# Optimization experiments

Measured on AMD Instinct MI355X. Metric: run time of the kernel, lower is better.

## Reference

```python
import jax, jax.numpy as jnp
import numpy as np


def setup_inputs() -> dict:
    key = jax.random.key(0)
    ks = jax.random.split(key, 7)
    B, C, H, W = 8, 256, 128, 128
    Cq = C // 8  # reduction_factor = 8
    x = jax.random.normal(ks[0], (B, C, H, W), jnp.float32)
    Wq = jax.random.normal(ks[1], (Cq, C), jnp.float32) * 0.05
    bq = jax.random.normal(ks[2], (Cq,), jnp.float32) * 0.01
    Wk = jax.random.normal(ks[3], (Cq, C), jnp.float32) * 0.05
    bk = jax.random.normal(ks[4], (Cq,), jnp.float32) * 0.01
    Wv = jax.random.normal(ks[5], (C, C), jnp.float32) * 0.05
    bv = jax.random.normal(ks[6], (C,), jnp.float32) * 0.01
    gamma = jnp.ones((1,), jnp.float32) * 0.5  # nonzero so attention path is active
    return {"x": x, "Wq": Wq, "bq": bq, "Wk": Wk, "bk": bk, "Wv": Wv, "bv": bv, "gamma": gamma}


def reference(x, Wq, bq, Wk, bk, Wv, bv, gamma):
    # 1x1 convs == per-pixel channel projections
    q = jnp.einsum('bchw,oc->bohw', x, Wq) + bq[None, :, None, None]  # [B,Cq,H,W]
    k = jnp.einsum('bchw,oc->bohw', x, Wk) + bk[None, :, None, None]
    v = jnp.einsum('bchw,oc->bohw', x, Wv) + bv[None, :, None, None]  # [B,C,H,W]

    H = x.shape[2]
    eye = jnp.eye(H, dtype=x.dtype)  # additive identity self-mask (note: +1, per source)

    # column (height) attention: for each (b, w), attend along h
    logit_h = jnp.einsum('bciw,bcjw->bwij', q, k) + eye  # [B,W,H,H]
    att_h = jax.nn.softmax(logit_h, axis=-1)
    out_h = jnp.einsum('bwij,bcjw->bciw', att_h, v)  # [B,C,H,W]

    # row (width) attention: for each (b, h), attend along w
    logit_w = jnp.einsum('bchi,bchj->bhij', q, k)  # [B,H,W,W]
    att_w = jax.nn.softmax(logit_w, axis=-1)
    out_w = jnp.einsum('bhij,bchj->bchi', att_w, v)  # [B,C,H,W]

    return gamma[0] * (out_h + out_w) + x
```

## Files before the change

kernel.cpp:

```cpp
#include <hip/hip_runtime.h>
#include <hip/hip_bf16.h>

#define BN 8
#define CN 256
#define CQn 32
#define HN 128
#define WN 128
#define LST 132

using bf16 = __hip_bfloat16;
typedef short short8 __attribute__((ext_vector_type(8)));
typedef float f32x4 __attribute__((ext_vector_type(4)));

__device__ __forceinline__ float ldf(const float* p) { return *p; }
__device__ __forceinline__ float ldf(const bf16* p) { return __bfloat162float(*p); }
__device__ __forceinline__ void stf(float* p, float v) { *p = v; }
__device__ __forceinline__ void stf(bf16* p, float v) { *p = __float2bfloat16(v); }
__device__ __forceinline__ unsigned short f2bu(float v) {
  bf16 h = __float2bfloat16(v);
  return *(unsigned short*)&h;
}
__device__ __forceinline__ float bu2f(unsigned short u) {
  return __bfloat162float(*(const bf16*)&u);
}
__device__ __forceinline__ unsigned pack2(float a, float b) {
  return (unsigned)f2bu(a) | ((unsigned)f2bu(b) << 16);
}
__device__ __forceinline__ uint4 add8bf16(uint4 a, uint4 b) {
  union { uint4 v; unsigned short u[8]; } A, B, C;
  A.v = a; B.v = b;
#pragma unroll
  for (int e = 0; e < 8; ++e) C.u[e] = f2bu(bu2f(A.u[e]) + bu2f(B.u[e]));
  return C.v;
}


__global__ __launch_bounds__(256) void proj_qk2(
    const float* __restrict__ x, const float* __restrict__ Wq, const float* __restrict__ bq,
    const float* __restrict__ Wk, const float* __restrict__ bk,
    bf16* __restrict__ qF, bf16* __restrict__ kF) {
  __shared__ float xs[64][128];
  __shared__ float wqs[CQn][64];
  __shared__ float wks[CQn][64];
  __shared__ float bqs[CQn], bks[CQn];
  const int tid = threadIdx.x;
  const int b = blockIdx.x >> 7, h = blockIdx.x & 127;
  if (tid < CQn) { bqs[tid] = bq[tid]; bks[tid] = bk[tid]; }
  const int w0 = (tid & 63) * 2;
  const int g = tid >> 6;
  float accq[8][2] = {};
  float acck[8][2] = {};
  for (int cc = 0; cc < CN; cc += 64) {
    __syncthreads();
    for (int idx = tid; idx < 64 * 128; idx += 256) {
      int c = idx >> 7, ww = idx & 127;
      xs[c][ww] = x[(((size_t)b * CN + cc + c) * HN + h) * WN + ww];
    }
    for (int idx = tid; idx < CQn * 64; idx += 256) {
      int oc = idx >> 6, c = idx & 63;
      wqs[oc][c] = Wq[oc * CN + cc + c];
      wks[oc][c] = Wk[oc * CN + cc + c];
    }
    __syncthreads();
    for (int c4 = 0; c4 < 64; c4 += 4) {
      float xa[4][2];
#pragma unroll
      for (int a = 0; a < 4; ++a) {
        float2 v = *(const float2*)&xs[c4 + a][w0];
        xa[a][0] = v.x; xa[a][1] = v.y;
      }
#pragma unroll
      for (int r = 0; r < 8; ++r) {
        float4 wq4 = *(const float4*)&wqs[g * 8 + r][c4];
        float4 wk4 = *(const float4*)&wks[g * 8 + r][c4];
        float wqa[4] = {wq4.x, wq4.y, wq4.z, wq4.w};
        float wka[4] = {wk4.x, wk4.y, wk4.z, wk4.w};
#pragma unroll
        for (int a = 0; a < 4; ++a) {
          accq[r][0] += wqa[a] * xa[a][0];
          accq[r][1] += wqa[a] * xa[a][1];
          acck[r][0] += wka[a] * xa[a][0];
          acck[r][1] += wka[a] * xa[a][1];
        }
      }
    }
  }
#pragma unroll
  for (int e = 0; e < 2; ++e) {
    union { unsigned short u[8]; uint4 v; } pq, pk;
#pragma unroll
    for (int rr = 0; rr < 8; ++rr) {
      int oc = g * 8 + rr;
      pq.u[rr] = f2bu(accq[rr][e] + bqs[oc]);
      pk.u[rr] = f2bu(acck[rr][e] + bks[oc]);
    }
    size_t base = (((size_t)b * 128 + h) * 128 + (w0 + e)) * 32 + g * 8;
    *(uint4*)&qF[base] = pq.v;
    *(uint4*)&kF[base] = pk.v;
  }
}

template <bool COL>
__global__ __launch_bounds__(256) void attn_mfma(
    const bf16* __restrict__ qF, const bf16* __restrict__ kF,
    const void* __restrict__ vsrc, bf16* __restrict__ outP) {
  __shared__ unsigned short psm[128 * 128];
  __shared__ float rsum[128];
  const int tid = threadIdx.x;
  const int wid = tid >> 6;
  const int lane = tid & 63;
  const int l15 = lane & 15, lg = lane >> 4;
  const int b = blockIdx.x >> 7, r = blockIdx.x & 127;

  short8 qf[2];
  const int ti0 = wid * 2;
#pragma unroll
  for (int t2 = 0; t2 < 2; ++t2) {
    int i = (ti0 + t2) * 16 + l15;
    size_t base = COL ? (((size_t)b * 128 + i) * 128 + r) * 32
                      : (((size_t)b * 128 + r) * 128 + i) * 32;
    qf[t2] = *(const short8*)&qF[base + lg * 8];
  }
  f32x4 lgt[2][8];
#pragma unroll
  for (int t2 = 0; t2 < 2; ++t2)
#pragma unroll
    for (int tj = 0; tj < 8; ++tj)
#pragma unroll
      for (int e = 0; e < 4; ++e) lgt[t2][tj][e] = 0.f;
#pragma unroll
  for (int tj = 0; tj < 8; ++tj) {
    int j = tj * 16 + l15;
    size_t base = COL ? (((size_t)b * 128 + j) * 128 + r) * 32
                      : (((size_t)b * 128 + r) * 128 + j) * 32;
    short8 kf = *(const short8*)&kF[base + lg * 8];
#pragma unroll
    for (int t2 = 0; t2 < 2; ++t2)
      lgt[t2][tj] = __builtin_amdgcn_mfma_f32_16x16x32_bf16(kf, qf[t2], lgt[t2][tj], 0, 0, 0);
  }

#pragma unroll
  for (int t2 = 0; t2 < 2; ++t2) {
    const int i = (ti0 + t2) * 16 + l15;
    if (COL) {
#pragma unroll
      for (int tj = 0; tj < 8; ++tj)
#pragma unroll
        for (int rr = 0; rr < 4; ++rr)
          if (tj * 16 + lg * 4 + rr == i) lgt[t2][tj][rr] += 1.0f;
    }
    float m = -1e30f;
#pragma unroll
    for (int tj = 0; tj < 8; ++tj)
#pragma unroll
      for (int rr = 0; rr < 4; ++rr) m = fmaxf(m, lgt[t2][tj][rr]);
    m = fmaxf(m, __shfl_xor(m, 16, 64));
    m = fmaxf(m, __shfl_xor(m, 32, 64));
    float s = 0.f;
#pragma unroll
    for (int tj = 0; tj < 8; ++tj)
#pragma unroll
      for (int rr = 0; rr < 4; ++rr) {
        float e = __expf(lgt[t2][tj][rr] - m);
        lgt[t2][tj][rr] = e;
        s += e;
      }
    s += __shfl_xor(s, 16, 64);
    s += __shfl_xor(s, 32, 64);
    if (lg == 0) rsum[i] = s;
#pragma unroll
    for (int tj = 0; tj < 8; ++tj) {
      int slot = ((tj * 2) + (lg >> 1)) ^ (i & 7);
      int elem = i * 128 + slot * 8 + (lg & 1) * 4;
      uint2 v;
      v.x = pack2(lgt[t2][tj][0], lgt[t2][tj][1]);
      v.y = pack2(lgt[t2][tj][2], lgt[t2][tj][3]);
      *(uint2*)&psm[elem] = v;
    }
  }
  __syncthreads();

  float rinv[8];
#pragma unroll
  for (int nt = 0; nt < 8; ++nt) rinv[nt] = 1.0f / rsum[nt * 16 + l15];

  const int cbase = wid * 64;
  const float* xf = (const float*)vsrc;
  const bf16* xb = (const bf16*)vsrc;
  unsigned short* ou = (unsigned short*)outP;
#pragma unroll
  for (int cp = 0; cp < 2; ++cp) {
    short8 vf[2][4];
#pragma unroll
    for (int u = 0; u < 2; ++u) {
      int c = cbase + (cp * 2 + u) * 16 + l15;
#pragma unroll
      for (int ks = 0; ks < 4; ++ks) {
        if (COL) {
          vf[u][ks] = *(const short8*)&xb[(((size_t)b * 256 + c) * 128 + r) * 128 + ks * 32 + lg * 8];
        } else {
          const float* xp = &xf[((size_t)b * 256 + c) * 16384 + r * 128 + ks * 32 + lg * 8];
          float4 f0 = *(const float4*)xp;
          float4 f1 = *(const float4*)(xp + 4);
          union { unsigned short u16[8]; short8 s8; } tmp;
          tmp.u16[0] = f2bu(f0.x); tmp.u16[1] = f2bu(f0.y);
          tmp.u16[2] = f2bu(f0.z); tmp.u16[3] = f2bu(f0.w);
          tmp.u16[4] = f2bu(f1.x); tmp.u16[5] = f2bu(f1.y);
          tmp.u16[6] = f2bu(f1.z); tmp.u16[7] = f2bu(f1.w);
          vf[u][ks] = tmp.s8;
        }
      }
    }
    f32x4 acc[2][8];
#pragma unroll
    for (int u = 0; u < 2; ++u)
#pragma unroll
      for (int nt = 0; nt < 8; ++nt)
#pragma unroll
        for (int e = 0; e < 4; ++e) acc[u][nt][e] = 0.f;
#pragma unroll
    for (int ks = 0; ks < 4; ++ks)
#pragma unroll
      for (int nt = 0; nt < 8; ++nt) {
        int i = nt * 16 + l15;
        short8 pf = *(const short8*)&psm[i * 128 + (((ks * 4) + lg) ^ (i & 7)) * 8];
#pragma unroll
        for (int u = 0; u < 2; ++u)
          acc[u][nt] = __builtin_amdgcn_mfma_f32_16x16x32_bf16(vf[u][ks], pf, acc[u][nt], 0, 0, 0);
      }
#pragma unroll
    for (int u = 0; u < 2; ++u) {
      int ct = cp * 2 + u;
      int cg = wid * 8 + ct * 2 + (lg >> 1);
#pragma unroll
      for (int nt = 0; nt < 8; ++nt) {
        int i = nt * 16 + l15;
        float sc = rinv[nt];
        uint2 v;
        v.x = pack2(acc[u][nt][0] * sc, acc[u][nt][1] * sc);
        v.y = pack2(acc[u][nt][2] * sc, acc[u][nt][3] * sc);
        size_t elem = ((((size_t)b * 32 + cg) * 128 + r) * 128 + i) * 8 + (lg & 1) * 4;
        *(uint2*)&ou[elem] = v;
      }
    }
  }
}

__global__ __launch_bounds__(256) void packed_merge2(const bf16* __restrict__ thP,
                                                     bf16* __restrict__ twP) {
  __shared__ uint4 ts[32][33];
  const int tid = threadIdx.x;
  const int blk = blockIdx.x;
  const int tI = blk & 15;
  const int cg = (blk >> 4) & 31;
  const int b = blk >> 9;
  const int h0 = (tI >> 2) * 32, w0 = (tI & 3) * 32;
  const uint4* tp = (const uint4*)thP;
  uint4* tw = (uint4*)twP;
#pragma unroll
  for (int rep = 0; rep < 4; ++rep) {
    int cell = rep * 256 + tid;
    int ww = cell >> 5, hh = cell & 31;
    ts[ww][hh] = tp[(((size_t)b * 32 + cg) * 128 + (w0 + ww)) * 128 + (h0 + hh)];
  }
  __syncthreads();
#pragma unroll
  for (int rep = 0; rep < 4; ++rep) {
    int cell = rep * 256 + tid;
    int hh = cell >> 5, ww = cell & 31;
    size_t o = (((size_t)b * 32 + cg) * 128 + (h0 + hh)) * 128 + (w0 + ww);
    tw[o] = add8bf16(tw[o], ts[ww][hh]);
  }
}


template <typename TIn>
__global__ __launch_bounds__(256) void transpose_bf16(const TIn* __restrict__ in,
                                                      bf16* __restrict__ out) {
  __shared__ float tile[32][33];
  const int blk = blockIdx.x;
  const int p = blk >> 4, t = blk & 15;
  const int r0 = (t >> 2) * 32, c0 = (t & 3) * 32;
  const int tx = threadIdx.x & 31, ty = threadIdx.x >> 5;
  const TIn* ip = in + (size_t)p * 128 * 128;
#pragma unroll
  for (int rr = 0; rr < 4; ++rr)
    tile[ty + 8 * rr][tx] = ldf(&ip[(r0 + ty + 8 * rr) * 128 + c0 + tx]);
  __syncthreads();
  bf16* op = out + (size_t)p * 128 * 128;
#pragma unroll
  for (int rr = 0; rr < 4; ++rr)
    op[(c0 + ty + 8 * rr) * 128 + r0 + tx] = __float2bfloat16(tile[tx][ty + 8 * rr]);
}

__global__ __launch_bounds__(256) void wv_to_bf16(const float* __restrict__ Wv,
                                                  bf16* __restrict__ Wvb) {
  int i = blockIdx.x * 256 + threadIdx.x;
  Wvb[i] = __float2bfloat16(Wv[i]);
}

__global__ __launch_bounds__(256) void proj_qk(
    const float* __restrict__ x, const float* __restrict__ Wq, const float* __restrict__ bq,
    const float* __restrict__ Wk, const float* __restrict__ bk,
    bf16* __restrict__ q, bf16* __restrict__ k) {
  __shared__ float xs[64][128];
  __shared__ float wqs[CQn][64];
  __shared__ float wks[CQn][64];
  __shared__ float bqs[CQn], bks[CQn];
  const int tid = threadIdx.x;
  const int b = blockIdx.x >> 7, h = blockIdx.x & 127;
  if (tid < CQn) { bqs[tid] = bq[tid]; bks[tid] = bk[tid]; }
  const int w0 = (tid & 63) * 2;
  const int g = tid >> 6;
  float accq[8][2] = {};
  float acck[8][2] = {};
  for (int cc = 0; cc < CN; cc += 64) {
    __syncthreads();
    for (int idx = tid; idx < 64 * 128; idx += 256) {
      int c = idx >> 7, ww = idx & 127;
      xs[c][ww] = x[(((size_t)b * CN + cc + c) * HN + h) * WN + ww];
    }
    for (int idx = tid; idx < CQn * 64; idx += 256) {
      int oc = idx >> 6, c = idx & 63;
      wqs[oc][c] = Wq[oc * CN + cc + c];
      wks[oc][c] = Wk[oc * CN + cc + c];
    }
    __syncthreads();
    for (int c4 = 0; c4 < 64; c4 += 4) {
      float xa[4][2];
#pragma unroll
      for (int a = 0; a < 4; ++a) {
        float2 v = *(const float2*)&xs[c4 + a][w0];
        xa[a][0] = v.x; xa[a][1] = v.y;
      }
#pragma unroll
      for (int r = 0; r < 8; ++r) {
        float4 wq4 = *(const float4*)&wqs[g * 8 + r][c4];
        float4 wk4 = *(const float4*)&wks[g * 8 + r][c4];
        float wqa[4] = {wq4.x, wq4.y, wq4.z, wq4.w};
        float wka[4] = {wk4.x, wk4.y, wk4.z, wk4.w};
#pragma unroll
        for (int a = 0; a < 4; ++a) {
          accq[r][0] += wqa[a] * xa[a][0];
          accq[r][1] += wqa[a] * xa[a][1];
          acck[r][0] += wka[a] * xa[a][0];
          acck[r][1] += wka[a] * xa[a][1];
        }
      }
    }
  }
#pragma unroll
  for (int r = 0; r < 8; ++r) {
    int oc = g * 8 + r;
    size_t off = (((size_t)b * CQn + oc) * HN + h) * WN + w0;
    q[off]     = __float2bfloat16(accq[r][0] + bqs[oc]);
    q[off + 1] = __float2bfloat16(accq[r][1] + bqs[oc]);
    k[off]     = __float2bfloat16(acck[r][0] + bks[oc]);
    k[off + 1] = __float2bfloat16(acck[r][1] + bks[oc]);
  }
}

template <typename XT, typename OT, bool ADD_EYE, bool PACKED>
__global__ __launch_bounds__(256) void attn_1d(
    const bf16* __restrict__ qsrc, const bf16* __restrict__ ksrc,
    const XT* __restrict__ xsrc, OT* __restrict__ outp) {
  extern __shared__ float sm[];
  float* qs  = sm;
  float* ks  = sm + 4096;
  float* Ls  = sm + 8192;
  float* xsv = sm + 8192 + 128 * LST;
  float* red = sm + 8192 + 160 * LST;
  float* rsum = sm + 8192 + 160 * LST + 256;
  const int tid = threadIdx.x;
  const int b = blockIdx.x >> 7, r = blockIdx.x & 127;

  for (int idx = tid; idx < CQn * 128; idx += 256) {
    int c = idx >> 7, j = idx & 127;
    size_t off = (((size_t)b * CQn + c) * 128 + r) * 128 + j;
    qs[idx] = __bfloat162float(qsrc[off]);
    ks[idx] = __bfloat162float(ksrc[off]);
  }
  __syncthreads();
#pragma unroll
  for (int g = 0; g < 4; ++g) {
    int t = tid + g * 256;
    int i0 = (t >> 5) * 4, j0 = (t & 31) * 4;
    float acc[4][4] = {};
    for (int c = 0; c < CQn; ++c) {
      float4 qv = *(const float4*)&qs[c * 128 + i0];
      float4 kv = *(const float4*)&ks[c * 128 + j0];
      float qa[4] = {qv.x, qv.y, qv.z, qv.w};
      float ka[4] = {kv.x, kv.y, kv.z, kv.w};
#pragma unroll
      for (int ii = 0; ii < 4; ++ii)
#pragma unroll
        for (int jj = 0; jj < 4; ++jj) acc[ii][jj] += qa[ii] * ka[jj];
    }
#pragma unroll
    for (int ii = 0; ii < 4; ++ii) {
      if (ADD_EYE) {
        int i = i0 + ii;
        if (i >= j0 && i < j0 + 4) acc[ii][i - j0] += 1.0f;
      }
      float4 o = make_float4(acc[ii][0], acc[ii][1], acc[ii][2], acc[ii][3]);
      *(float4*)&Ls[(i0 + ii) * LST + j0] = o;
    }
  }
  __syncthreads();
  {
    const int row = tid & 127, jb = (tid >> 7) * 64;
    float m = -1e30f;
    for (int j = 0; j < 64; ++j) m = fmaxf(m, Ls[row * LST + jb + j]);
    red[tid] = m;
    __syncthreads();
    m = fmaxf(red[row], red[row + 128]);
    float s = 0.f;
    for (int j = 0; j < 64; ++j) {
      float e = __expf(Ls[row * LST + jb + j] - m);
      Ls[row * LST + jb + j] = e;
      s += e;
    }
    __syncthreads();
    red[tid] = s;
    __syncthreads();
    if (tid < 128) rsum[tid] = red[tid] + red[tid + 128];
  }
  const int ci0 = (tid >> 5) * 4;
  const int il = tid & 31;
  float rinv[4];
  __syncthreads();
#pragma unroll
  for (int a = 0; a < 4; ++a) rinv[a] = 1.0f / rsum[il + 32 * a];

  for (int cc0 = 0; cc0 < CN; cc0 += 32) {
    __syncthreads();
    for (int idx = tid; idx < 32 * 128; idx += 256) {
      int c = idx >> 7, j = idx & 127;
      xsv[c * LST + j] = ldf(&xsrc[(((size_t)b * CN + cc0 + c) * 128 + r) * 128 + j]);
    }
    __syncthreads();
    float acc[4][4] = {};
    for (int j0 = 0; j0 < 128; j0 += 4) {
      float xa[4][4], pa[4][4];
#pragma unroll
      for (int ci = 0; ci < 4; ++ci) {
        float4 v = *(const float4*)&xsv[(ci0 + ci) * LST + j0];
        xa[ci][0] = v.x; xa[ci][1] = v.y; xa[ci][2] = v.z; xa[ci][3] = v.w;
      }
#pragma unroll
      for (int a = 0; a < 4; ++a) {
        float4 v = *(const float4*)&Ls[(il + 32 * a) * LST + j0];
        pa[a][0] = v.x; pa[a][1] = v.y; pa[a][2] = v.z; pa[a][3] = v.w;
      }
#pragma unroll
      for (int ci = 0; ci < 4; ++ci)
#pragma unroll
        for (int a = 0; a < 4; ++a)
          acc[ci][a] += xa[ci][0] * pa[a][0] + xa[ci][1] * pa[a][1] +
                        xa[ci][2] * pa[a][2] + xa[ci][3] * pa[a][3];
    }
    if constexpr (PACKED) {
      __syncthreads();
      unsigned short* xu = (unsigned short*)xsv;
#pragma unroll
      for (int ci = 0; ci < 4; ++ci)
#pragma unroll
        for (int a = 0; a < 4; ++a)
          xu[(ci0 + ci) * 132 + il + 32 * a] = f2bu(acc[ci][a] * rinv[a]);
      __syncthreads();
      unsigned short* ou = (unsigned short*)outp;
#pragma unroll
      for (int p = 0; p < 2; ++p) {
        int idx = p * 256 + tid;
        int cgL = idx >> 7, px = idx & 127;
        unsigned short tmp[8];
#pragma unroll
        for (int e = 0; e < 8; ++e) tmp[e] = xu[(cgL * 8 + e) * 132 + px];
        size_t g16 = (((size_t)b * 32 + (cc0 >> 3) + cgL) * 128 + r) * 128 + px;
        *(uint4*)&ou[g16 * 8] = *(const uint4*)tmp;
      }
    } else {
#pragma unroll
      for (int ci = 0; ci < 4; ++ci) {
        size_t base = (((size_t)b * CN + cc0 + ci0 + ci) * 128 + r) * 128 + il;
#pragma unroll
        for (int a = 0; a < 4; ++a) stf(&outp[base + 32 * a], acc[ci][a] * rinv[a]);
      }
    }
  }
}

__global__ __launch_bounds__(256) void packed_merge(const bf16* __restrict__ thT,
                                                    bf16* __restrict__ twP) {
  __shared__ unsigned short ths[8 * 32 * 36];
  const int tid = threadIdx.x;
  const int blk = blockIdx.x;
  const int tI = blk & 15;
  const int cgI = (blk >> 4) & 31;
  const int b = blk >> 9;
  const int w0 = (tI >> 2) * 32, h0 = (tI & 3) * 32;
  {
    const int e = tid >> 5, ww = tid & 31;
    const unsigned short* src = (const unsigned short*)(thT +
        ((((size_t)b * 256 + cgI * 8 + e) * 128) + (w0 + ww)) * 128 + h0);
    unsigned short* dst = &ths[(e * 32 + ww) * 36];
#pragma unroll
    for (int j = 0; j < 8; ++j)
      *(uint2*)&dst[j * 4] = *(const uint2*)&src[j * 4];
  }
  __syncthreads();
  unsigned short* twu = (unsigned short*)twP;
#pragma unroll
  for (int rep = 0; rep < 4; ++rep) {
    int cell = rep * 256 + tid;
    int hh = cell >> 5, ww = cell & 31;
    size_t g16 = ((((size_t)b * 32 + cgI) * 128) + h0 + hh) * 128 + (w0 + ww);
    uint4 cur = *(const uint4*)&twu[g16 * 8];
    unsigned short cu[8];
    *(uint4*)cu = cur;
#pragma unroll
    for (int e = 0; e < 8; ++e)
      cu[e] = f2bu(bu2f(cu[e]) + bu2f(ths[(e * 32 + ww) * 36 + hh]));
    *(uint4*)&twu[g16 * 8] = *(const uint4*)cu;
  }
}

__global__ __launch_bounds__(512) void final_mfma(
    const bf16* __restrict__ twP, const bf16* __restrict__ Wvb,
    const float* __restrict__ x, const float* __restrict__ bv,
    const float* __restrict__ gamma, float* __restrict__ out) {
  __shared__ short As[256][64];
  __shared__ short Bs[128][64];
  const int tid = threadIdx.x;
  const int b = blockIdx.x >> 7, h = blockIdx.x & 127;
  const int lane = tid & 63;
  const int wid = tid >> 6;
  const int wm = wid >> 1, wn = wid & 1;
  const int l15 = lane & 15, lg = lane >> 4;
  const unsigned short* twu = (const unsigned short*)twP;

  f32x4 acc[4][4];
#pragma unroll
  for (int m = 0; m < 4; ++m)
#pragma unroll
    for (int n = 0; n < 4; ++n)
#pragma unroll
      for (int e = 0; e < 4; ++e) acc[m][n][e] = 0.f;

  for (int k0 = 0; k0 < 256; k0 += 64) {
    __syncthreads();
#pragma unroll
    for (int p = 0; p < 4; ++p) {
      int idx = p * 512 + tid;
      int co = idx >> 3, cg = idx & 7;
      uint4 v = *(const uint4*)&Wvb[(size_t)co * 256 + k0 + cg * 8];
      *(uint4*)&As[co][(cg ^ (co & 7)) * 8] = v;
    }
#pragma unroll
    for (int p = 0; p < 2; ++p) {
      int idx = p * 512 + tid;
      int w = idx & 127, cgL = idx >> 7;
      size_t g16 = (((size_t)b * 32 + (k0 >> 3) + cgL) * 128 + h) * 128 + w;
      uint4 v = *(const uint4*)&twu[g16 * 8];
      *(uint4*)&Bs[w][(cgL ^ (w & 7)) * 8] = v;
    }
    __syncthreads();
    short8 a[4][2], bb[4][2];
#pragma unroll
    for (int m = 0; m < 4; ++m)
#pragma unroll
      for (int kk = 0; kk < 2; ++kk) {
        int co = wm * 64 + m * 16 + l15;
        int cg = kk * 4 + lg;
        a[m][kk] = *(const short8*)&As[co][(cg ^ (co & 7)) * 8];
      }
#pragma unroll
    for (int n = 0; n < 4; ++n)
#pragma unroll
      for (int kk = 0; kk < 2; ++kk) {
        int w = wn * 64 + n * 16 + l15;
        int cg = kk * 4 + lg;
        bb[n][kk] = *(const short8*)&Bs[w][(cg ^ (w & 7)) * 8];
      }
#pragma unroll
    for (int kk = 0; kk < 2; ++kk)
#pragma unroll
      for (int m = 0; m < 4; ++m)
#pragma unroll
        for (int n = 0; n < 4; ++n)
          acc[m][n] = __builtin_amdgcn_mfma_f32_16x16x32_bf16(a[m][kk], bb[n][kk], acc[m][n], 0, 0, 0);
  }

  const float g = gamma[0];
  float bvv[4][4];
#pragma unroll
  for (int m = 0; m < 4; ++m)
#pragma unroll
    for (int rr = 0; rr < 4; ++rr)
      bvv[m][rr] = 2.0f * bv[wm * 64 + m * 16 + lg * 4 + rr];
#pragma unroll
  for (int m = 0; m < 4; ++m)
#pragma unroll
    for (int n = 0; n < 4; ++n) {
      int w = wn * 64 + n * 16 + l15;
#pragma unroll
      for (int rr = 0; rr < 4; ++rr) {
        int co = wm * 64 + m * 16 + lg * 4 + rr;
        size_t o = (((size_t)b * 256 + co) * 128 + h) * 128 + w;
        out[o] = g * (acc[m][n][rr] + bvv[m][rr]) + x[o];
      }
    }
}

extern "C" void kernel_launch(void* const* d_in, const int* in_sizes, int n_in,
                              void* d_out, int out_size, void* d_ws, size_t ws_size,
                              hipStream_t stream) {
  const float* x     = (const float*)d_in[0];
  const float* Wq    = (const float*)d_in[1];
  const float* bq    = (const float*)d_in[2];
  const float* Wk    = (const float*)d_in[3];
  const float* bk    = (const float*)d_in[4];
  const float* Wv    = (const float*)d_in[5];
  const float* bv    = (const float*)d_in[6];
  const float* gamma = (const float*)d_in[7];
  float* out = (float*)d_out;

  const size_t QSZ = (size_t)BN * CQn * HN * WN;
  const size_t XSZ = (size_t)BN * CN * HN * WN;
  bf16* wsb = (bf16*)d_ws;

  const size_t need3 = (2 * QSZ + 3 * XSZ + 65536) * sizeof(bf16);
  const size_t need2 = (4 * QSZ + 2 * XSZ + 65536) * sizeof(bf16);

  if (ws_size >= need3) {
    bf16* qF  = wsb;
    bf16* kF  = wsb + QSZ;
    bf16* xT  = wsb + 2 * QSZ;
    bf16* twP = wsb + 2 * QSZ + XSZ;
    bf16* thP = wsb + 2 * QSZ + 2 * XSZ;
    bf16* Wvb = wsb + 2 * QSZ + 3 * XSZ;
    proj_qk2<<<BN * HN, 256, 0, stream>>>(x, Wq, bq, Wk, bk, qF, kF);
    transpose_bf16<float><<<BN * CN * 16, 256, 0, stream>>>(x, xT);
    wv_to_bf16<<<256, 256, 0, stream>>>(Wv, Wvb);
    attn_mfma<false><<<BN * HN, 256, 0, stream>>>(qF, kF, (const void*)x, twP);
    attn_mfma<true><<<BN * WN, 256, 0, stream>>>(qF, kF, (const void*)xT, thP);
    packed_merge2<<<BN * 32 * 16, 256, 0, stream>>>(thP, twP);
    final_mfma<<<BN * HN, 512, 0, stream>>>(twP, Wvb, x, bv, gamma, out);
  } else if (ws_size >= need2) {
    bf16* q   = wsb;
    bf16* k   = wsb + QSZ;
    bf16* qT  = wsb + 2 * QSZ;
    bf16* kT  = wsb + 3 * QSZ;
    bf16* xT  = wsb + 4 * QSZ;
    bf16* twP = wsb + 4 * QSZ + XSZ;
    bf16* Wvb = wsb + 4 * QSZ + 2 * XSZ;
    const int ATTN_LDS = (8192 + 160 * LST + 384) * 4;
    auto* fa_row_pk = attn_1d<float, bf16, false, true>;
    auto* fa_col    = attn_1d<bf16, bf16, true, false>;
    hipFuncSetAttribute((const void*)fa_row_pk, hipFuncAttributeMaxDynamicSharedMemorySize, ATTN_LDS);
    hipFuncSetAttribute((const void*)fa_col,    hipFuncAttributeMaxDynamicSharedMemorySize, ATTN_LDS);
    proj_qk<<<BN * HN, 256, 0, stream>>>(x, Wq, bq, Wk, bk, q, k);
    transpose_bf16<bf16><<<2 * BN * CQn * 16, 256, 0, stream>>>(q, qT);
    transpose_bf16<float><<<BN * CN * 16, 256, 0, stream>>>(x, xT);
    wv_to_bf16<<<256, 256, 0, stream>>>(Wv, Wvb);
    fa_row_pk<<<BN * HN, 256, ATTN_LDS, stream>>>(q, k, x, twP);
    fa_col<<<BN * WN, 256, ATTN_LDS, stream>>>(qT, kT, xT, xT);
    packed_merge<<<BN * 32 * 16, 256, 0, stream>>>(xT, twP);
    final_mfma<<<BN * HN, 512, 0, stream>>>(twP, Wvb, x, bv, gamma, out);
  } else {
    hipMemsetAsync(d_out, 0x7f, (size_t)out_size * sizeof(float), stream);
  }
}
```

Before: 300.7 us.

## Use MFMA for Q/K projection and emit bf16 copy of x for reuse

The scalar FP32 Q/K projection becomes a bf16 MFMA kernel that splits each row into two halves. While it loads x, it also writes a bf16 copy of x. That copy feeds the row attention directly and is the source for the transpose, so the later kernels read bf16 instead of fp32. The thP buffer now reuses the xbf workspace after the row attention has consumed it, and the fallback path with the old kernels is removed. The change trades some projection precision (bf16 inputs) for less fp32 traffic and faster projection compute.

```diff
diff --git a/kernel.cpp b/kernel.cpp
--- a/kernel.cpp
+++ b/kernel.cpp
@@ -6,7 +6,6 @@
 #define CQn 32
 #define HN 128
 #define WN 128
-#define LST 132
 
 using bf16 = __hip_bfloat16;
 typedef short short8 __attribute__((ext_vector_type(8)));
@@ -14,8 +13,6 @@
 
 __device__ __forceinline__ float ldf(const float* p) { return *p; }
 __device__ __forceinline__ float ldf(const bf16* p) { return __bfloat162float(*p); }
-__device__ __forceinline__ void stf(float* p, float v) { *p = v; }
-__device__ __forceinline__ void stf(bf16* p, float v) { *p = __float2bfloat16(v); }
 __device__ __forceinline__ unsigned short f2bu(float v) {
   bf16 h = __float2bfloat16(v);
   return *(unsigned short*)&h;
@@ -34,76 +31,114 @@
   return C.v;
 }
 
-
-__global__ __launch_bounds__(256) void proj_qk2(
+__global__ __launch_bounds__(256) void proj_qk3(
     const float* __restrict__ x, const float* __restrict__ Wq, const float* __restrict__ bq,
     const float* __restrict__ Wk, const float* __restrict__ bk,
-    bf16* __restrict__ qF, bf16* __restrict__ kF) {
-  __shared__ float xs[64][128];
-  __shared__ float wqs[CQn][64];
-  __shared__ float wks[CQn][64];
-  __shared__ float bqs[CQn], bks[CQn];
+    bf16* __restrict__ qF, bf16* __restrict__ kF, bf16* __restrict__ xbf) {
+  __shared__ unsigned short xs[256 * 64];
+  __shared__ unsigned short Ws[64 * 256];
   const int tid = threadIdx.x;
-  const int b = blockIdx.x >> 7, h = blockIdx.x & 127;
-  if (tid < CQn) { bqs[tid] = bq[tid]; bks[tid] = bk[tid]; }
-  const int w0 = (tid & 63) * 2;
-  const int g = tid >> 6;
-  float accq[8][2] = {};
-  float acck[8][2] = {};
-  for (int cc = 0; cc < CN; cc += 64) {
-    __syncthreads();
-    for (int idx = tid; idx < 64 * 128; idx += 256) {
-      int c = idx >> 7, ww = idx & 127;
-      xs[c][ww] = x[(((size_t)b * CN + cc + c) * HN + h) * WN + ww];
-    }
-    for (int idx = tid; idx < CQn * 64; idx += 256) {
-      int oc = idx >> 6, c = idx & 63;
-      wqs[oc][c] = Wq[oc * CN + cc + c];
-      wks[oc][c] = Wk[oc * CN + cc + c];
-    }
-    __syncthreads();
-    for (int c4 = 0; c4 < 64; c4 += 4) {
-      float xa[4][2];
-#pragma unroll
-      for (int a = 0; a < 4; ++a) {
-        float2 v = *(const float2*)&xs[c4 + a][w0];
-        xa[a][0] = v.x; xa[a][1] = v.y;
-      }
-#pragma unroll
-      for (int r = 0; r < 8; ++r) {
-        float4 wq4 = *(const float4*)&wqs[g * 8 + r][c4];
-        float4 wk4 = *(const float4*)&wks[g * 8 + r][c4];
-        float wqa[4] = {wq4.x, wq4.y, wq4.z, wq4.w};
-        float wka[4] = {wk4.x, wk4.y, wk4.z, wk4.w};
-#pragma unroll
-        for (int a = 0; a < 4; ++a) {
-          accq[r][0] += wqa[a] * xa[a][0];
-          accq[r][1] += wqa[a] * xa[a][1];
-          acck[r][0] += wka[a] * xa[a][0];
-          acck[r][1] += wka[a] * xa[a][1];
-        }
-      }
-    }
-  }
-#pragma unroll
-  for (int e = 0; e < 2; ++e) {
-    union { unsigned short u[8]; uint4 v; } pq, pk;
-#pragma unroll
-    for (int rr = 0; rr < 8; ++rr) {
-      int oc = g * 8 + rr;
-      pq.u[rr] = f2bu(accq[rr][e] + bqs[oc]);
-      pk.u[rr] = f2bu(acck[rr][e] + bks[oc]);
-    }
-    size_t base = (((size_t)b * 128 + h) * 128 + (w0 + e)) * 32 + g * 8;
-    *(uint4*)&qF[base] = pq.v;
-    *(uint4*)&kF[base] = pk.v;
-  }
+  const int half = blockIdx.x & 1;
+  const int bh = blockIdx.x >> 1;
+  const int b = bh >> 7, h = bh & 127;
+  const int w0 = half * 64;
+
+#pragma unroll
+  for (int it = 0; it < 8; ++it) {
+    int idx = it * 256 + tid;
+    int oc = idx >> 5, cg = idx & 31;
+    const float* wp = (oc < 32) ? &Wq[(size_t)oc * 256 + cg * 8]
+                                : &Wk[(size_t)(oc - 32) * 256 + cg * 8];
+    float4 f0 = *(const float4*)wp;
+    float4 f1 = *(const float4*)(wp + 4);
+    union { unsigned short u[8]; uint4 v; } t;
+    t.u[0] = f2bu(f0.x); t.u[1] = f2bu(f0.y); t.u[2] = f2bu(f0.z); t.u[3] = f2bu(f0.w);
+    t.u[4] = f2bu(f1.x); t.u[5] = f2bu(f1.y); t.u[6] = f2bu(f1.z); t.u[7] = f2bu(f1.w);
+    *(uint4*)&Ws[oc * 256 + (cg ^ (oc & 7)) * 8] = t.v;
+  }
+  unsigned short* xbu = (unsigned short*)xbf;
+#pragma unroll
+  for (int it = 0; it < 16; ++it) {
+    int idx = it * 256 + tid;
+    int c = idx >> 4, wc = idx & 15;
+    size_t gix = (((size_t)b * 256 + c) * 128 + h) * 128 + w0 + wc * 4;
+    float4 f = *(const float4*)&x[gix];
+    union { unsigned short u[4]; uint2 v; } t;
+    t.u[0] = f2bu(f.x); t.u[1] = f2bu(f.y); t.u[2] = f2bu(f.z); t.u[3] = f2bu(f.w);
+    *(uint2*)&xs[c * 64 + wc * 4] = t.v;
+    *(uint2*)&xbu[gix] = t.v;
+  }
+  __syncthreads();
+
+  const int lane = tid & 63, wid = tid >> 6;
+  const int l15 = lane & 15, lg = lane >> 4;
+  f32x4 acc[4];
+#pragma unroll
+  for (int mt = 0; mt < 4; ++mt)
+#pragma unroll
+    for (int e = 0; e < 4; ++e) acc[mt][e] = 0.f;
+
+#pragma unroll
+  for (int ks = 0; ks < 8; ++ks) {
+    union { unsigned short u[8]; short8 s; } bf;
+#pragma unroll
+    for (int e = 0; e < 8; ++e)
+      bf.u[e] = xs[(ks * 32 + lg * 8 + e) * 64 + wid * 16 + l15];
+#pragma unroll
+    for (int mt = 0; mt < 4; ++mt) {
+      int oc = mt * 16 + l15;
+      short8 af = *(const short8*)&Ws[oc * 256 + ((ks * 4 + lg) ^ (oc & 7)) * 8];
+      acc[mt] = __builtin_amdgcn_mfma_f32_16x16x32_bf16(af, bf.s, acc[mt], 0, 0, 0);
+    }
+  }
+
+  const int w = w0 + wid * 16 + l15;
+#pragma unroll
+  for (int mt = 0; mt < 4; ++mt) {
+    float bb[4];
+#pragma unroll
+    for (int rr = 0; rr < 4; ++rr) {
+      int ch = (mt & 1) * 16 + lg * 4 + rr;
+      bb[rr] = (mt < 2) ? bq[ch] : bk[ch];
+    }
+    uint2 v;
+    v.x = pack2(acc[mt][0] + bb[0], acc[mt][1] + bb[1]);
+    v.y = pack2(acc[mt][2] + bb[2], acc[mt][3] + bb[3]);
+    size_t base = (((size_t)b * 128 + h) * 128 + w) * 32 + (mt & 1) * 16 + lg * 4;
+    if (mt < 2) *(uint2*)&((unsigned short*)qF)[base] = v;
+    else        *(uint2*)&((unsigned short*)kF)[base] = v;
+  }
+}
+
+template <typename TIn>
+__global__ __launch_bounds__(256) void transpose_bf16(const TIn* __restrict__ in,
+                                                      bf16* __restrict__ out) {
+  __shared__ float tile[32][33];
+  const int blk = blockIdx.x;
+  const int p = blk >> 4, t = blk & 15;
+  const int r0 = (t >> 2) * 32, c0 = (t & 3) * 32;
+  const int tx = threadIdx.x & 31, ty = threadIdx.x >> 5;
+  const TIn* ip = in + (size_t)p * 128 * 128;
+#pragma unroll
+  for (int rr = 0; rr < 4; ++rr)
+    tile[ty + 8 * rr][tx] = ldf(&ip[(r0 + ty + 8 * rr) * 128 + c0 + tx]);
+  __syncthreads();
+  bf16* op = out + (size_t)p * 128 * 128;
+#pragma unroll
+  for (int rr = 0; rr < 4; ++rr)
+    op[(c0 + ty + 8 * rr) * 128 + r0 + tx] = __float2bfloat16(tile[tx][ty + 8 * rr]);
+}
+
+__global__ __launch_bounds__(256) void wv_to_bf16(const float* __restrict__ Wv,
+                                                  bf16* __restrict__ Wvb) {
+  int i = blockIdx.x * 256 + threadIdx.x;
+  Wvb[i] = __float2bfloat16(Wv[i]);
 }
 
 template <bool COL>
 __global__ __launch_bounds__(256) void attn_mfma(
     const bf16* __restrict__ qF, const bf16* __restrict__ kF,
-    const void* __restrict__ vsrc, bf16* __restrict__ outP) {
+    const bf16* __restrict__ vsrc, bf16* __restrict__ outP) {
   __shared__ unsigned short psm[128 * 128];
   __shared__ float rsum[128];
   const int tid = threadIdx.x;
@@ -185,8 +220,6 @@
   for (int nt = 0; nt < 8; ++nt) rinv[nt] = 1.0f / rsum[nt * 16 + l15];
 
   const int cbase = wid * 64;
-  const float* xf = (const float*)vsrc;
-  const bf16* xb = (const bf16*)vsrc;
   unsigned short* ou = (unsigned short*)outP;
 #pragma unroll
   for (int cp = 0; cp < 2; ++cp) {
@@ -195,21 +228,8 @@
     for (int u = 0; u < 2; ++u) {
       int c = cbase + (cp * 2 + u) * 16 + l15;
 #pragma unroll
-      for (int ks = 0; ks < 4; ++ks) {
-        if (COL) {
-          vf[u][ks] = *(const short8*)&xb[(((size_t)b * 256 + c) * 128 + r) * 128 + ks * 32 + lg * 8];
-        } else {
-          const float* xp = &xf[((size_t)b * 256 + c) * 16384 + r * 128 + ks * 32 + lg * 8];
-          float4 f0 = *(const float4*)xp;
-          float4 f1 = *(const float4*)(xp + 4);
-          union { unsigned short u16[8]; short8 s8; } tmp;
-          tmp.u16[0] = f2bu(f0.x); tmp.u16[1] = f2bu(f0.y);
-          tmp.u16[2] = f2bu(f0.z); tmp.u16[3] = f2bu(f0.w);
-          tmp.u16[4] = f2bu(f1.x); tmp.u16[5] = f2bu(f1.y);
-          tmp.u16[6] = f2bu(f1.z); tmp.u16[7] = f2bu(f1.w);
-          vf[u][ks] = tmp.s8;
-        }
-      }
+      for (int ks = 0; ks < 4; ++ks)
+        vf[u][ks] = *(const short8*)&vsrc[(((size_t)b * 256 + c) * 128 + r) * 128 + ks * 32 + lg * 8];
     }
     f32x4 acc[2][8];
 #pragma unroll
@@ -270,258 +290,6 @@
     int hh = cell >> 5, ww = cell & 31;
     size_t o = (((size_t)b * 32 + cg) * 128 + (h0 + hh)) * 128 + (w0 + ww);
     tw[o] = add8bf16(tw[o], ts[ww][hh]);
-  }
-}
-
-
-template <typename TIn>
-__global__ __launch_bounds__(256) void transpose_bf16(const TIn* __restrict__ in,
-                                                      bf16* __restrict__ out) {
-  __shared__ float tile[32][33];
-  const int blk = blockIdx.x;
-  const int p = blk >> 4, t = blk & 15;
-  const int r0 = (t >> 2) * 32, c0 = (t & 3) * 32;
-  const int tx = threadIdx.x & 31, ty = threadIdx.x >> 5;
-  const TIn* ip = in + (size_t)p * 128 * 128;
-#pragma unroll
-  for (int rr = 0; rr < 4; ++rr)
-    tile[ty + 8 * rr][tx] = ldf(&ip[(r0 + ty + 8 * rr) * 128 + c0 + tx]);
-  __syncthreads();
-  bf16* op = out + (size_t)p * 128 * 128;
-#pragma unroll
-  for (int rr = 0; rr < 4; ++rr)
-    op[(c0 + ty + 8 * rr) * 128 + r0 + tx] = __float2bfloat16(tile[tx][ty + 8 * rr]);
-}
-
-__global__ __launch_bounds__(256) void wv_to_bf16(const float* __restrict__ Wv,
-                                                  bf16* __restrict__ Wvb) {
-  int i = blockIdx.x * 256 + threadIdx.x;
-  Wvb[i] = __float2bfloat16(Wv[i]);
-}
-
-__global__ __launch_bounds__(256) void proj_qk(
-    const float* __restrict__ x, const float* __restrict__ Wq, const float* __restrict__ bq,
-    const float* __restrict__ Wk, const float* __restrict__ bk,
-    bf16* __restrict__ q, bf16* __restrict__ k) {
-  __shared__ float xs[64][128];
-  __shared__ float wqs[CQn][64];
-  __shared__ float wks[CQn][64];
-  __shared__ float bqs[CQn], bks[CQn];
-  const int tid = threadIdx.x;
-  const int b = blockIdx.x >> 7, h = blockIdx.x & 127;
-  if (tid < CQn) { bqs[tid] = bq[tid]; bks[tid] = bk[tid]; }
-  const int w0 = (tid & 63) * 2;
-  const int g = tid >> 6;
-  float accq[8][2] = {};
-  float acck[8][2] = {};
-  for (int cc = 0; cc < CN; cc += 64) {
-    __syncthreads();
-    for (int idx = tid; idx < 64 * 128; idx += 256) {
-      int c = idx >> 7, ww = idx & 127;
-      xs[c][ww] = x[(((size_t)b * CN + cc + c) * HN + h) * WN + ww];
-    }
-    for (int idx = tid; idx < CQn * 64; idx += 256) {
-      int oc = idx >> 6, c = idx & 63;
-      wqs[oc][c] = Wq[oc * CN + cc + c];
-      wks[oc][c] = Wk[oc * CN + cc + c];
-    }
-    __syncthreads();
-    for (int c4 = 0; c4 < 64; c4 += 4) {
-      float xa[4][2];
-#pragma unroll
-      for (int a = 0; a < 4; ++a) {
-        float2 v = *(const float2*)&xs[c4 + a][w0];
-        xa[a][0] = v.x; xa[a][1] = v.y;
-      }
-#pragma unroll
-      for (int r = 0; r < 8; ++r) {
-        float4 wq4 = *(const float4*)&wqs[g * 8 + r][c4];
-        float4 wk4 = *(const float4*)&wks[g * 8 + r][c4];
-        float wqa[4] = {wq4.x, wq4.y, wq4.z, wq4.w};
-        float wka[4] = {wk4.x, wk4.y, wk4.z, wk4.w};
-#pragma unroll
-        for (int a = 0; a < 4; ++a) {
-          accq[r][0] += wqa[a] * xa[a][0];
-          accq[r][1] += wqa[a] * xa[a][1];
-          acck[r][0] += wka[a] * xa[a][0];
-          acck[r][1] += wka[a] * xa[a][1];
-        }
-      }
-    }
-  }
-#pragma unroll
-  for (int r = 0; r < 8; ++r) {
-    int oc = g * 8 + r;
-    size_t off = (((size_t)b * CQn + oc) * HN + h) * WN + w0;
-    q[off]     = __float2bfloat16(accq[r][0] + bqs[oc]);
-    q[off + 1] = __float2bfloat16(accq[r][1] + bqs[oc]);
-    k[off]     = __float2bfloat16(acck[r][0] + bks[oc]);
-    k[off + 1] = __float2bfloat16(acck[r][1] + bks[oc]);
-  }
-}
-
-template <typename XT, typename OT, bool ADD_EYE, bool PACKED>
-__global__ __launch_bounds__(256) void attn_1d(
-    const bf16* __restrict__ qsrc, const bf16* __restrict__ ksrc,
-    const XT* __restrict__ xsrc, OT* __restrict__ outp) {
-  extern __shared__ float sm[];
-  float* qs  = sm;
-  float* ks  = sm + 4096;
-  float* Ls  = sm + 8192;
-  float* xsv = sm + 8192 + 128 * LST;
-  float* red = sm + 8192 + 160 * LST;
-  float* rsum = sm + 8192 + 160 * LST + 256;
-  const int tid = threadIdx.x;
-  const int b = blockIdx.x >> 7, r = blockIdx.x & 127;
-
-  for (int idx = tid; idx < CQn * 128; idx += 256) {
-    int c = idx >> 7, j = idx & 127;
-    size_t off = (((size_t)b * CQn + c) * 128 + r) * 128 + j;
-    qs[idx] = __bfloat162float(qsrc[off]);
-    ks[idx] = __bfloat162float(ksrc[off]);
-  }
-  __syncthreads();
-#pragma unroll
-  for (int g = 0; g < 4; ++g) {
-    int t = tid + g * 256;
-    int i0 = (t >> 5) * 4, j0 = (t & 31) * 4;
-    float acc[4][4] = {};
-    for (int c = 0; c < CQn; ++c) {
-      float4 qv = *(const float4*)&qs[c * 128 + i0];
-      float4 kv = *(const float4*)&ks[c * 128 + j0];
-      float qa[4] = {qv.x, qv.y, qv.z, qv.w};
-      float ka[4] = {kv.x, kv.y, kv.z, kv.w};
-#pragma unroll
-      for (int ii = 0; ii < 4; ++ii)
-#pragma unroll
-        for (int jj = 0; jj < 4; ++jj) acc[ii][jj] += qa[ii] * ka[jj];
-    }
-#pragma unroll
-    for (int ii = 0; ii < 4; ++ii) {
-      if (ADD_EYE) {
-        int i = i0 + ii;
-        if (i >= j0 && i < j0 + 4) acc[ii][i - j0] += 1.0f;
-      }
-      float4 o = make_float4(acc[ii][0], acc[ii][1], acc[ii][2], acc[ii][3]);
-      *(float4*)&Ls[(i0 + ii) * LST + j0] = o;
-    }
-  }
-  __syncthreads();
-  {
-    const int row = tid & 127, jb = (tid >> 7) * 64;
-    float m = -1e30f;
-    for (int j = 0; j < 64; ++j) m = fmaxf(m, Ls[row * LST + jb + j]);
-    red[tid] = m;
-    __syncthreads();
-    m = fmaxf(red[row], red[row + 128]);
-    float s = 0.f;
-    for (int j = 0; j < 64; ++j) {
-      float e = __expf(Ls[row * LST + jb + j] - m);
-      Ls[row * LST + jb + j] = e;
-      s += e;
-    }
-    __syncthreads();
-    red[tid] = s;
-    __syncthreads();
-    if (tid < 128) rsum[tid] = red[tid] + red[tid + 128];
-  }
-  const int ci0 = (tid >> 5) * 4;
-  const int il = tid & 31;
-  float rinv[4];
-  __syncthreads();
-#pragma unroll
-  for (int a = 0; a < 4; ++a) rinv[a] = 1.0f / rsum[il + 32 * a];
-
-  for (int cc0 = 0; cc0 < CN; cc0 += 32) {
-    __syncthreads();
-    for (int idx = tid; idx < 32 * 128; idx += 256) {
-      int c = idx >> 7, j = idx & 127;
-      xsv[c * LST + j] = ldf(&xsrc[(((size_t)b * CN + cc0 + c) * 128 + r) * 128 + j]);
-    }
-    __syncthreads();
-    float acc[4][4] = {};
-    for (int j0 = 0; j0 < 128; j0 += 4) {
-      float xa[4][4], pa[4][4];
-#pragma unroll
-      for (int ci = 0; ci < 4; ++ci) {
-        float4 v = *(const float4*)&xsv[(ci0 + ci) * LST + j0];
-        xa[ci][0] = v.x; xa[ci][1] = v.y; xa[ci][2] = v.z; xa[ci][3] = v.w;
-      }
-#pragma unroll
-      for (int a = 0; a < 4; ++a) {
-        float4 v = *(const float4*)&Ls[(il + 32 * a) * LST + j0];
-        pa[a][0] = v.x; pa[a][1] = v.y; pa[a][2] = v.z; pa[a][3] = v.w;
-      }
-#pragma unroll
-      for (int ci = 0; ci < 4; ++ci)
-#pragma unroll
-        for (int a = 0; a < 4; ++a)
-          acc[ci][a] += xa[ci][0] * pa[a][0] + xa[ci][1] * pa[a][1] +
-                        xa[ci][2] * pa[a][2] + xa[ci][3] * pa[a][3];
-    }
-    if constexpr (PACKED) {
-      __syncthreads();
-      unsigned short* xu = (unsigned short*)xsv;
-#pragma unroll
-      for (int ci = 0; ci < 4; ++ci)
-#pragma unroll
-        for (int a = 0; a < 4; ++a)
-          xu[(ci0 + ci) * 132 + il + 32 * a] = f2bu(acc[ci][a] * rinv[a]);
-      __syncthreads();
-      unsigned short* ou = (unsigned short*)outp;
-#pragma unroll
-      for (int p = 0; p < 2; ++p) {
-        int idx = p * 256 + tid;
-        int cgL = idx >> 7, px = idx & 127;
-        unsigned short tmp[8];
-#pragma unroll
-        for (int e = 0; e < 8; ++e) tmp[e] = xu[(cgL * 8 + e) * 132 + px];
-        size_t g16 = (((size_t)b * 32 + (cc0 >> 3) + cgL) * 128 + r) * 128 + px;
-        *(uint4*)&ou[g16 * 8] = *(const uint4*)tmp;
-      }
-    } else {
-#pragma unroll
-      for (int ci = 0; ci < 4; ++ci) {
-        size_t base = (((size_t)b * CN + cc0 + ci0 + ci) * 128 + r) * 128 + il;
-#pragma unroll
-        for (int a = 0; a < 4; ++a) stf(&outp[base + 32 * a], acc[ci][a] * rinv[a]);
-      }
-    }
-  }
-}
-
-__global__ __launch_bounds__(256) void packed_merge(const bf16* __restrict__ thT,
-                                                    bf16* __restrict__ twP) {
-  __shared__ unsigned short ths[8 * 32 * 36];
-  const int tid = threadIdx.x;
-  const int blk = blockIdx.x;
-  const int tI = blk & 15;
-  const int cgI = (blk >> 4) & 31;
-  const int b = blk >> 9;
-  const int w0 = (tI >> 2) * 32, h0 = (tI & 3) * 32;
-  {
-    const int e = tid >> 5, ww = tid & 31;
-    const unsigned short* src = (const unsigned short*)(thT +
-        ((((size_t)b * 256 + cgI * 8 + e) * 128) + (w0 + ww)) * 128 + h0);
-    unsigned short* dst = &ths[(e * 32 + ww) * 36];
-#pragma unroll
-    for (int j = 0; j < 8; ++j)
-      *(uint2*)&dst[j * 4] = *(const uint2*)&src[j * 4];
-  }
-  __syncthreads();
-  unsigned short* twu = (unsigned short*)twP;
-#pragma unroll
-  for (int rep = 0; rep < 4; ++rep) {
-    int cell = rep * 256 + tid;
-    int hh = cell >> 5, ww = cell & 31;
-    size_t g16 = ((((size_t)b * 32 + cgI) * 128) + h0 + hh) * 128 + (w0 + ww);
-    uint4 cur = *(const uint4*)&twu[g16 * 8];
-    unsigned short cu[8];
-    *(uint4*)cu = cur;
-#pragma unroll
-    for (int e = 0; e < 8; ++e)
-      cu[e] = f2bu(bu2f(cu[e]) + bu2f(ths[(e * 32 + ww) * 36 + hh]));
-    *(uint4*)&twu[g16 * 8] = *(const uint4*)cu;
   }
 }
 
@@ -625,49 +393,29 @@
   const float* gamma = (const float*)d_in[7];
   float* out = (float*)d_out;
 
-  const size_t QSZ = (size_t)BN * CQn * HN * WN;
+  const size_t QSZ = (size_t)BN * HN * WN * CQn;
   const size_t XSZ = (size_t)BN * CN * HN * WN;
   bf16* wsb = (bf16*)d_ws;
 
-  const size_t need3 = (2 * QSZ + 3 * XSZ + 65536) * sizeof(bf16);
-  const size_t need2 = (4 * QSZ + 2 * XSZ + 65536) * sizeof(bf16);
-
-  if (ws_size >= need3) {
-    bf16* qF  = wsb;
-    bf16* kF  = wsb + QSZ;
-    bf16* xT  = wsb + 2 * QSZ;
-    bf16* twP = wsb + 2 * QSZ + XSZ;
-    bf16* thP = wsb + 2 * QSZ + 2 * XSZ;
-    bf16* Wvb = wsb + 2 * QSZ + 3 * XSZ;
-    proj_qk2<<<BN * HN, 256, 0, stream>>>(x, Wq, bq, Wk, bk, qF, kF);
-    transpose_bf16<float><<<BN * CN * 16, 256, 0, stream>>>(x, xT);
-    wv_to_bf16<<<256, 256, 0, stream>>>(Wv, Wvb);
-    attn_mfma<false><<<BN * HN, 256, 0, stream>>>(qF, kF, (const void*)x, twP);
-    attn_mfma<true><<<BN * WN, 256, 0, stream>>>(qF, kF, (const void*)xT, thP);
-    packed_merge2<<<BN * 32 * 16, 256, 0, stream>>>(thP, twP);
-    final_mfma<<<BN * HN, 512, 0, stream>>>(twP, Wvb, x, bv, gamma, out);
-  } else if (ws_size >= need2) {
-    bf16* q   = wsb;
-    bf16* k   = wsb + QSZ;
-    bf16* qT  = wsb + 2 * QSZ;
-    bf16* kT  = wsb + 3 * QSZ;
-    bf16* xT  = wsb + 4 * QSZ;
-    bf16* twP = wsb + 4 * QSZ + XSZ;
-    bf16* Wvb = wsb + 4 * QSZ + 2 * XSZ;
-    const int ATTN_LDS = (8192 + 160 * LST + 384) * 4;
-    auto* fa_row_pk = attn_1d<float, bf16, false, true>;
-    auto* fa_col    = attn_1d<bf16, bf16, true, false>;
-    hipFuncSetAttribute((const void*)fa_row_pk, hipFuncAttributeMaxDynamicSharedMemorySize, ATTN_LDS);
-    hipFuncSetAttribute((const void*)fa_col,    hipFuncAttributeMaxDynamicSharedMemorySize, ATTN_LDS);
-    proj_qk<<<BN * HN, 256, 0, stream>>>(x, Wq, bq, Wk, bk, q, k);
-    transpose_bf16<bf16><<<2 * BN * CQn * 16, 256, 0, stream>>>(q, qT);
-    transpose_bf16<float><<<BN * CN * 16, 256, 0, stream>>>(x, xT);
-    wv_to_bf16<<<256, 256, 0, stream>>>(Wv, Wvb);
-    fa_row_pk<<<BN * HN, 256, ATTN_LDS, stream>>>(q, k, x, twP);
-    fa_col<<<BN * WN, 256, ATTN_LDS, stream>>>(qT, kT, xT, xT);
-    packed_merge<<<BN * 32 * 16, 256, 0, stream>>>(xT, twP);
-    final_mfma<<<BN * HN, 512, 0, stream>>>(twP, Wvb, x, bv, gamma, out);
-  } else {
+  const size_t need = (2 * QSZ + 3 * XSZ + 65536) * sizeof(bf16);
+  if (ws_size < need) {
     hipMemsetAsync(d_out, 0x7f, (size_t)out_size * sizeof(float), stream);
-  }
-}
+    return;
+  }
+
+  bf16* qF  = wsb;
+  bf16* kF  = wsb + QSZ;
+  bf16* xbf = wsb + 2 * QSZ;
+  bf16* xT  = wsb + 2 * QSZ + XSZ;
+  bf16* twP = wsb + 2 * QSZ + 2 * XSZ;
+  bf16* Wvb = wsb + 2 * QSZ + 3 * XSZ;
+  bf16* thP = xbf;
+
+  proj_qk3<<<2 * BN * HN, 256, 0, stream>>>(x, Wq, bq, Wk, bk, qF, kF, xbf);
+  wv_to_bf16<<<256, 256, 0, stream>>>(Wv, Wvb);
+  transpose_bf16<bf16><<<BN * CN * 16, 256, 0, stream>>>(xbf, xT);
+  attn_mfma<false><<<BN * HN, 256, 0, stream>>>(qF, kF, xbf, twP);
+  attn_mfma<true><<<BN * WN, 256, 0, stream>>>(qF, kF, xT, thP);
+  packed_merge2<<<BN * 32 * 16, 256, 0, stream>>>(thP, twP);
+  final_mfma<<<BN * HN, 512, 0, stream>>>(twP, Wvb, x, bv, gamma, out);
+}
```

Result: faster. 246.4 us (-18.1%).
